# Kernel tuning notes

Measured on AMD Instinct MI355X. Metric: run time of the kernel, lower is better.

## Reference

```python
import jax, jax.numpy as jnp
import numpy as np
from jax import lax

B, L, D_MODEL = 4, 512, 256
N_LAYERS = 6
EXPAND = 2
D_INNER = EXPAND * D_MODEL  # 512
D_STATE = 16
D_CONV = 4
DT_RANK = (D_MODEL + 15) // 16  # 16
EPS = 1e-5


def silu(x):
    return x * jax.nn.sigmoid(x)


def rmsnorm(x, w):
    var = jnp.mean(x * x, axis=-1, keepdims=True)
    return x * lax.rsqrt(var + EPS) * w


def setup_inputs() -> dict:
    key = jax.random.key(0)
    ks = jax.random.split(key, 12)
    s = lambda *sh: 0.02
    inp = {
        "x": jax.random.normal(ks[0], (B, L, D_MODEL), dtype=jnp.float32),
        "norm_w": jnp.ones((N_LAYERS, D_MODEL), jnp.float32),
        "W_in": jax.random.normal(ks[1], (N_LAYERS, 2 * D_INNER, D_MODEL), jnp.float32) * 0.02,
        "b_in": jnp.zeros((N_LAYERS, 2 * D_INNER), jnp.float32),
        "conv_w": jax.random.normal(ks[2], (N_LAYERS, D_INNER, D_CONV), jnp.float32) * 0.2,
        "W_x": jax.random.normal(ks[3], (N_LAYERS, DT_RANK + 2 * D_STATE, D_INNER), jnp.float32) * 0.02,
        "dt_w": jax.random.normal(ks[4], (N_LAYERS, D_INNER, DT_RANK), jnp.float32) * 0.1,
        "dt_b": jax.random.uniform(ks[5], (N_LAYERS, D_INNER), jnp.float32, -4.0, -2.0),
        "A_log": jnp.log(jnp.broadcast_to(jnp.arange(1, D_STATE + 1, dtype=jnp.float32), (N_LAYERS, D_INNER, D_STATE))),
        "D": jnp.ones((N_LAYERS, D_INNER), jnp.float32),
        "W_out": jax.random.normal(ks[6], (N_LAYERS, D_MODEL, D_INNER), jnp.float32) * 0.02,
        "b_out": jnp.zeros((N_LAYERS, D_MODEL), jnp.float32),
    }
    return inp


def mamba_block(x, W_in, b_in, conv_w, W_x, dt_w, dt_b, A_log, D, W_out, b_out):
    # input projection -> (B, L, 2*d_inner)
    xz = jnp.einsum("bld,ed->ble", x, W_in) + b_in
    xin, z = xz[..., :D_INNER], xz[..., D_INNER:]
    # depthwise causal conv over time (groups = d_inner, left pad d_conv-1)
    xc = lax.conv_general_dilated(
        xin.transpose(0, 2, 1),            # (B, C, L)
        conv_w[:, None, :],                # (C, 1, K)
        window_strides=(1,),
        padding=[(D_CONV - 1, 0)],
        feature_group_count=D_INNER,
        dimension_numbers=("NCH", "OIH", "NCH"),
    ).transpose(0, 2, 1)
    u = silu(xc)                           # (B, L, d_inner)
    # data-dependent dt, B, C
    xdbc = jnp.einsum("bld,rd->blr", u, W_x)
    dt = xdbc[..., :DT_RANK]
    Bm = xdbc[..., DT_RANK:DT_RANK + D_STATE]
    Cm = xdbc[..., DT_RANK + D_STATE:]
    delta = jax.nn.softplus(jnp.einsum("blr,dr->bld", dt, dt_w) + dt_b)
    A = -jnp.exp(A_log)                    # (d_inner, d_state)
    dA = jnp.exp(jnp.einsum("bld,dn->bldn", delta, A))
    dBu = jnp.einsum("bld,bln->bldn", delta * u, Bm)
    # selective scan over time
    def step(h, inp):
        dA_t, dBu_t, C_t = inp
        h = dA_t * h + dBu_t               # (B, d_inner, d_state)
        y_t = jnp.einsum("bdn,bn->bd", h, C_t)
        return h, y_t
    h0 = jnp.zeros((B, D_INNER, D_STATE), x.dtype)
    _, ys = lax.scan(step, h0, (dA.transpose(1, 0, 2, 3), dBu.transpose(1, 0, 2, 3), Cm.transpose(1, 0, 2)))
    y = ys.transpose(1, 0, 2) + u * D      # skip connection D*u
    y = y * silu(z)
    return jnp.einsum("bld,md->blm", y, W_out) + b_out


def reference(x, norm_w, W_in, b_in, conv_w, W_x, dt_w, dt_b, A_log, D, W_out, b_out):
    for i in range(N_LAYERS):
        x = x + mamba_block(rmsnorm(x, norm_w[i]), W_in[i], b_in[i], conv_w[i], W_x[i], dt_w[i], dt_b[i], A_log[i], D[i], W_out[i], b_out[i])
    return x
```

## Files before the change

### kernel.cpp

```cpp
#include <hip/hip_runtime.h>
#include <hip/hip_bf16.h>

#define B_SZ 4
#define L_SZ 512
#define D_MODEL 256
#define D_INNER 512
#define D_STATE 16
#define DT_RANK 16
#define N_LAYERS 6
#define BL (B_SZ * L_SZ)

typedef __bf16 bf16_t;
typedef __bf16 bf16x8 __attribute__((ext_vector_type(8)));
typedef __bf16 bf16x4 __attribute__((ext_vector_type(4)));
typedef float  f32x4  __attribute__((ext_vector_type(4)));

__device__ __forceinline__ float row_allreduce16(float x)
{
    int v;
    v = __builtin_amdgcn_mov_dpp(__float_as_int(x), 0x121, 0xf, 0xf, true);
    x += __int_as_float(v);
    v = __builtin_amdgcn_mov_dpp(__float_as_int(x), 0x122, 0xf, 0xf, true);
    x += __int_as_float(v);
    v = __builtin_amdgcn_mov_dpp(__float_as_int(x), 0x124, 0xf, 0xf, true);
    x += __int_as_float(v);
    v = __builtin_amdgcn_mov_dpp(__float_as_int(x), 0x128, 0xf, 0xf, true);
    x += __int_as_float(v);
    return x;
}

__global__ __launch_bounds__(256) void cast3_kernel(
    const float* __restrict__ s0, const float* __restrict__ s1,
    const float* __restrict__ s2, bf16_t* __restrict__ dst,
    int n0, int n1, int n2)
{
    int i = blockIdx.x * 256 + threadIdx.x;
    const float* s; int off;
    if (i < n0)            { s = s0; off = i; }
    else if (i < n0 + n1)  { s = s1; off = i - n0; }
    else if (i < n0+n1+n2) { s = s2; off = i - n0 - n1; }
    else return;
    const float4 v = *(const float4*)(s + (size_t)off * 4);
    bf16x4 o;
    o[0] = (bf16_t)v.x; o[1] = (bf16_t)v.y;
    o[2] = (bf16_t)v.z; o[3] = (bf16_t)v.w;
    *(bf16x4*)(dst + (size_t)i * 4) = o;
}

__global__ __launch_bounds__(256) void rmsnorm_kernel(
    const float* __restrict__ x, const float* __restrict__ w,
    bf16_t* __restrict__ o)
{
    int row  = blockIdx.x * 4 + (threadIdx.x >> 6);
    int lane = threadIdx.x & 63;
    const float4 v = *(const float4*)(x + (size_t)row * D_MODEL + lane * 4);
    float ss = v.x * v.x + v.y * v.y + v.z * v.z + v.w * v.w;
    #pragma unroll
    for (int off = 32; off; off >>= 1) ss += __shfl_xor(ss, off);
    float rs = rsqrtf(ss * (1.f / D_MODEL) + 1e-5f);
    const float4 wv = *(const float4*)(w + lane * 4);
    bf16x4 ov;
    ov[0] = (bf16_t)(v.x * rs * wv.x);
    ov[1] = (bf16_t)(v.y * rs * wv.y);
    ov[2] = (bf16_t)(v.z * rs * wv.z);
    ov[3] = (bf16_t)(v.w * rs * wv.w);
    *(bf16x4*)(o + (size_t)row * D_MODEL + lane * 4) = ov;
}

__global__ __launch_bounds__(256) void win_kernel(
    const bf16_t* __restrict__ A,
    const bf16_t* __restrict__ Bw,
    const float* __restrict__ bias,
    float* __restrict__ C,
    float* __restrict__ Z)
{
    constexpr int K = 256, BK = 64;
    __shared__ bf16_t As[64][K + 8];
    __shared__ bf16_t Bs[64][BK + 8];

    const int tid  = threadIdx.x;
    const int wave = tid >> 6, lane = tid & 63;
    const int wm = wave >> 1, wn = wave & 1;
    const int lm = lane & 15, quad = lane >> 4;
    const int m0 = blockIdx.y * 64, n0 = blockIdx.x * 64;

    #pragma unroll
    for (int i = tid; i < 64 * (K / 8); i += 256) {
        int r = i >> 5, c8 = i & 31;
        *(bf16x8*)&As[r][c8 * 8] =
            *(const bf16x8*)(A + (size_t)(m0 + r) * K + c8 * 8);
    }

    f32x4 acc[2][2] = {};
    for (int k0 = 0; k0 < K; k0 += BK) {
        #pragma unroll
        for (int i = tid; i < 64 * (BK / 8); i += 256) {
            int r = i >> 3, c8 = i & 7;
            *(bf16x8*)&Bs[r][c8 * 8] =
                *(const bf16x8*)(Bw + (size_t)(n0 + r) * K + k0 + c8 * 8);
        }
        __syncthreads();
        #pragma unroll
        for (int ks = 0; ks < 2; ++ks) {
            bf16x8 af[2], bfr[2];
            #pragma unroll
            for (int i = 0; i < 2; ++i)
                af[i] = *(const bf16x8*)&As[wm * 32 + i * 16 + lm][k0 + ks * 32 + quad * 8];
            #pragma unroll
            for (int j = 0; j < 2; ++j)
                bfr[j] = *(const bf16x8*)&Bs[wn * 32 + j * 16 + lm][ks * 32 + quad * 8];
            #pragma unroll
            for (int i = 0; i < 2; ++i)
                #pragma unroll
                for (int j = 0; j < 2; ++j)
                    acc[i][j] = __builtin_amdgcn_mfma_f32_16x16x32_bf16(
                        af[i], bfr[j], acc[i][j], 0, 0, 0);
        }
        __syncthreads();
    }

    if (n0 >= D_INNER) {
        #pragma unroll
        for (int i = 0; i < 2; ++i) {
            int rowbase = m0 + wm * 32 + i * 16 + quad * 4;
            #pragma unroll
            for (int j = 0; j < 2; ++j) {
                int col = n0 + wn * 32 + j * 16 + lm;
                float4 o;
                #pragma unroll
                for (int r = 0; r < 4; ++r) {
                    float v = acc[i][j][r] + bias[col];
                    ((float*)&o)[r] = v / (1.f + __expf(-v));
                }
                *(float4*)(Z + (size_t)(col - D_INNER) * BL + rowbase) = o;
            }
        }
        return;
    }

    #pragma unroll
    for (int i = 0; i < 2; ++i) {
        #pragma unroll
        for (int j = 0; j < 2; ++j) {
            int col = n0 + wn * 32 + j * 16 + lm;
            #pragma unroll
            for (int r = 0; r < 4; ++r) {
                int rowm = m0 + wm * 32 + i * 16 + quad * 4 + r;
                C[(size_t)rowm * D_INNER + col] = acc[i][j][r] + bias[col];
            }
        }
    }
}

template<int WM, int WN, int TM_T, int TN_T>
__global__ __launch_bounds__(64 * WM * WN) void gemm_wout(
    const bf16_t* __restrict__ A, int lda,
    const bf16_t* __restrict__ Bw, int ldb,
    const float* __restrict__ bias,
    const float* __restrict__ R, int ldr,
    float* __restrict__ C, int ldc, int K)
{
    constexpr int BK = 64;
    constexpr int BM = WM * TM_T * 16;
    constexpr int BN = WN * TN_T * 16;
    constexpr int NT = 64 * WM * WN;
    constexpr int LDK = BK + 8;
    __shared__ bf16_t As[BM][LDK];
    __shared__ bf16_t Bs[BN][LDK];

    const int tid  = threadIdx.x;
    const int wave = tid >> 6, lane = tid & 63;
    const int wm = wave / WN, wn = wave % WN;
    const int lm = lane & 15, quad = lane >> 4;
    const int m0 = blockIdx.y * BM, n0 = blockIdx.x * BN;

    f32x4 acc[TM_T][TN_T] = {};

    for (int k0 = 0; k0 < K; k0 += BK) {
        #pragma unroll
        for (int i = tid; i < BM * (BK / 8); i += NT) {
            int r = i >> 3, c8 = i & 7;
            *(bf16x8*)&As[r][c8 * 8] =
                *(const bf16x8*)(A + (size_t)(m0 + r) * lda + k0 + c8 * 8);
        }
        #pragma unroll
        for (int i = tid; i < BN * (BK / 8); i += NT) {
            int r = i >> 3, c8 = i & 7;
            *(bf16x8*)&Bs[r][c8 * 8] =
                *(const bf16x8*)(Bw + (size_t)(n0 + r) * ldb + k0 + c8 * 8);
        }
        __syncthreads();
        #pragma unroll
        for (int ks = 0; ks < BK / 32; ++ks) {
            bf16x8 af[TM_T], bfr[TN_T];
            #pragma unroll
            for (int i = 0; i < TM_T; ++i)
                af[i] = *(const bf16x8*)&As[wm * TM_T * 16 + i * 16 + lm][ks * 32 + quad * 8];
            #pragma unroll
            for (int j = 0; j < TN_T; ++j)
                bfr[j] = *(const bf16x8*)&Bs[wn * TN_T * 16 + j * 16 + lm][ks * 32 + quad * 8];
            #pragma unroll
            for (int i = 0; i < TM_T; ++i)
                #pragma unroll
                for (int j = 0; j < TN_T; ++j)
                    acc[i][j] = __builtin_amdgcn_mfma_f32_16x16x32_bf16(
                        af[i], bfr[j], acc[i][j], 0, 0, 0);
        }
        __syncthreads();
    }

    #pragma unroll
    for (int i = 0; i < TM_T; ++i) {
        #pragma unroll
        for (int j = 0; j < TN_T; ++j) {
            int col = n0 + wn * TN_T * 16 + j * 16 + lm;
            #pragma unroll
            for (int r = 0; r < 4; ++r) {
                int rowm = m0 + wm * TM_T * 16 + i * 16 + quad * 4 + r;
                C[(size_t)rowm * ldc + col] =
                    acc[i][j][r] + bias[col] + R[(size_t)rowm * ldr + col];
            }
        }
    }
}

__global__ __launch_bounds__(256) void wx_conv_kernel(
    const float* __restrict__ xzx,
    const float* __restrict__ cw,
    const bf16_t* __restrict__ Bw,
    const float* __restrict__ dt_w,
    const float* __restrict__ dt_b,
    float* __restrict__ uT,
    float* __restrict__ xdbcT,
    float* __restrict__ deltaT)
{
    constexpr int K = 512;
    __shared__ float  xs[19][516];
    __shared__ bf16_t us[16][520];
    __shared__ f32x4  part[4][3][64];
    __shared__ float  dtt[16][17];

    const int tid  = threadIdx.x;
    const int wave = tid >> 6, lane = tid & 63;
    const int lm = lane & 15, quad = lane >> 4;
    const int m0 = blockIdx.x * 16;

    for (int q = tid; q < 19 * 128; q += 256) {
        int rx = q >> 7, c4 = (q & 127) * 4;
        int mr = m0 - 3 + rx;
        float4 v = make_float4(0.f, 0.f, 0.f, 0.f);
        if (mr >= 0) v = *(const float4*)(xzx + (size_t)mr * K + c4);
        *(float4*)&xs[rx][c4] = v;
    }
    __syncthreads();

    #pragma unroll
    for (int it = 0; it < 8; ++it) {
        int item = tid + it * 256;
        int d = item >> 2, rg = item & 3;
        const float4 wv = *(const float4*)(cw + d * 4);
        float4 o;
        #pragma unroll
        for (int e = 0; e < 4; ++e) {
            int ro = rg * 4 + e;
            int t  = (m0 + ro) & (L_SZ - 1);
            float a = wv.w * xs[ro + 3][d];
            if (t >= 1) a += wv.z * xs[ro + 2][d];
            if (t >= 2) a += wv.y * xs[ro + 1][d];
            if (t >= 3) a += wv.x * xs[ro + 0][d];
            a = a / (1.f + __expf(-a));
            ((float*)&o)[e] = a;
            us[ro][d] = (bf16_t)a;
        }
        *(float4*)(uT + (size_t)d * BL + m0 + rg * 4) = o;
    }
    __syncthreads();

    f32x4 acc[3] = {};
    const int kb = wave * 128 + quad * 8;
    #pragma unroll
    for (int ks = 0; ks < 4; ++ks) {
        int k0 = kb + ks * 32;
        bf16x8 af = *(const bf16x8*)&us[lm][k0];
        #pragma unroll
        for (int j = 0; j < 3; ++j) {
            bf16x8 bfr = *(const bf16x8*)(Bw + (size_t)(j * 16 + lm) * K + k0);
            acc[j] = __builtin_amdgcn_mfma_f32_16x16x32_bf16(af, bfr, acc[j], 0, 0, 0);
        }
    }
    #pragma unroll
    for (int j = 0; j < 3; ++j) part[wave][j][lane] = acc[j];
    __syncthreads();

    if (tid < 192) {
        int j = tid >> 6, l = tid & 63;
        f32x4 s = part[0][j][l];
        s += part[1][j][l];
        s += part[2][j][l];
        s += part[3][j][l];
        int col = j * 16 + (l & 15);
        float4 v = make_float4(s[0], s[1], s[2], s[3]);
        *(float4*)(xdbcT + (size_t)col * BL + m0 + (l >> 4) * 4) = v;
        if (j == 0) {
            #pragma unroll
            for (int e = 0; e < 4; ++e)
                dtt[(l >> 4) * 4 + e][l & 15] = s[e];
        }
    }
    __syncthreads();

    #pragma unroll
    for (int it = 0; it < 8; ++it) {
        int item = tid + it * 256;
        int d = item >> 2, tg = item & 3;
        const float4 w0 = *(const float4*)(dt_w + (size_t)d * 16 + 0);
        const float4 w1 = *(const float4*)(dt_w + (size_t)d * 16 + 4);
        const float4 w2 = *(const float4*)(dt_w + (size_t)d * 16 + 8);
        const float4 w3 = *(const float4*)(dt_w + (size_t)d * 16 + 12);
        const float bdt = dt_b[d];
        float4 o;
        #pragma unroll
        for (int e = 0; e < 4; ++e) {
            int t = tg * 4 + e;
            float a = bdt;
            a += dtt[t][0]  * w0.x + dtt[t][1]  * w0.y + dtt[t][2]  * w0.z + dtt[t][3]  * w0.w;
            a += dtt[t][4]  * w1.x + dtt[t][5]  * w1.y + dtt[t][6]  * w1.z + dtt[t][7]  * w1.w;
            a += dtt[t][8]  * w2.x + dtt[t][9]  * w2.y + dtt[t][10] * w2.z + dtt[t][11] * w2.w;
            a += dtt[t][12] * w3.x + dtt[t][13] * w3.y + dtt[t][14] * w3.z + dtt[t][15] * w3.w;
            ((float*)&o)[e] = (a > 20.f) ? a : __logf(1.f + __expf(a));
        }
        *(float4*)(deltaT + (size_t)d * BL + m0 + tg * 4) = o;
    }
}

__global__ __launch_bounds__(1024, 4) void scan_kernel(
    const float* __restrict__ xdbcT,
    const float* __restrict__ deltaT,
    const float* __restrict__ uT,
    const float* __restrict__ szT,
    const float* __restrict__ A_log,
    const float* __restrict__ Dv,
    bf16_t* __restrict__ y)
{
    constexpr int TC = 32;
    constexpr int NW = L_SZ / TC;

    int blk  = blockIdx.x;
    int b    = blk >> 7;
    int dg   = blk & 127;
    int wave = threadIdx.x >> 6;
    int lane = threadIdx.x & 63;
    int d    = dg * 4 + (lane >> 4);
    int n    = lane & 15;

    __shared__ float lds_Ap[NW][64];
    __shared__ float lds_he[NW][64];

    float Adn = -__expf(A_log[d * D_STATE + n]);
    int r0 = b * L_SZ + wave * TC;

    const float* Brow = xdbcT  + (size_t)(DT_RANK + n) * BL;
    const float* Crow = xdbcT  + (size_t)(DT_RANK + D_STATE + n) * BL;
    const float* drow = deltaT + (size_t)d * BL;
    const float* urow = uT     + (size_t)d * BL;
    const float* zrow = szT    + (size_t)d * BL;

    {
        float h = 0.f, P = 1.f;
        #pragma unroll
        for (int j4 = 0; j4 < 8; ++j4) {
            int rb = r0 + j4 * 4;
            f32x4 dl = *(const f32x4*)(drow + rb);
            f32x4 Bv = *(const f32x4*)(Brow + rb);
            f32x4 uv = *(const f32x4*)(urow + rb);
            #pragma unroll
            for (int k = 0; k < 4; ++k) {
                float dA = __expf(dl[k] * Adn);
                h = dA * h + dl[k] * uv[k] * Bv[k];
                P *= dA;
            }
        }
        lds_Ap[wave][lane] = P;
        lds_he[wave][lane] = h;
    }
    __syncthreads();

    float H = 0.f;
    for (int j = 0; j < wave; ++j)
        H = lds_Ap[j][lane] * H + lds_he[j][lane];

    float Dd = Dv[d];
    float h = H;
    #pragma unroll
    for (int g = 0; g < 2; ++g) {
        float py[16];
        #pragma unroll
        for (int j4 = 0; j4 < 4; ++j4) {
            int rb = r0 + g * 16 + j4 * 4;
            f32x4 dl = *(const f32x4*)(drow + rb);
            f32x4 Bv = *(const f32x4*)(Brow + rb);
            f32x4 uv = *(const f32x4*)(urow + rb);
            f32x4 Cc = *(const f32x4*)(Crow + rb);
            #pragma unroll
            for (int k = 0; k < 4; ++k) {
                float dA = __expf(dl[k] * Adn);
                h = dA * h + dl[k] * uv[k] * Bv[k];
                py[j4 * 4 + k] = h * Cc[k];
            }
        }
        #pragma unroll
        for (int j = 0; j < 16; ++j)
            py[j] = row_allreduce16(py[j]);
        if (n == 0) {
            #pragma unroll
            for (int j4 = 0; j4 < 4; ++j4) {
                int rb = r0 + g * 16 + j4 * 4;
                f32x4 uv = *(const f32x4*)(urow + rb);
                f32x4 sz = *(const f32x4*)(zrow + rb);
                #pragma unroll
                for (int k = 0; k < 4; ++k) {
                    int row = rb + k;
                    y[(size_t)row * D_INNER + d] =
                        (bf16_t)((py[j4*4+k] + uv[k] * Dd) * sz[k]);
                }
            }
        }
    }
}

extern "C" void kernel_launch(void* const* d_in, const int* in_sizes, int n_in,
                              void* d_out, int out_size, void* d_ws, size_t ws_size,
                              hipStream_t stream)
{
    const float* x_in   = (const float*)d_in[0];
    const float* norm_w = (const float*)d_in[1];
    const float* W_in   = (const float*)d_in[2];
    const float* b_in   = (const float*)d_in[3];
    const float* conv_w = (const float*)d_in[4];
    const float* W_x    = (const float*)d_in[5];
    const float* dt_w   = (const float*)d_in[6];
    const float* dt_b   = (const float*)d_in[7];
    const float* A_log  = (const float*)d_in[8];
    const float* Dv     = (const float*)d_in[9];
    const float* W_out  = (const float*)d_in[10];
    const float* b_out  = (const float*)d_in[11];
    float* out = (float*)d_out;

    float* ws     = (float*)d_ws;
    float* xz     = ws;
    float* uT     = xz     + BL * D_INNER;
    float* szT    = uT     + D_INNER * BL;
    float* xdbcT  = szT    + D_INNER * BL;
    float* deltaT = xdbcT  + 48 * BL;
    bf16_t* bws   = (bf16_t*)(deltaT + D_INNER * BL);
    bf16_t* xn_bf = bws;
    bf16_t* y_bf  = xn_bf + BL * D_MODEL;
    bf16_t* Wi_bf = y_bf  + BL * D_INNER;
    bf16_t* Wx_bf = Wi_bf + N_LAYERS * 2 * D_INNER * D_MODEL;
    bf16_t* Wo_bf = Wx_bf + N_LAYERS * 48 * D_INNER;

    {
        int n0 = N_LAYERS * 2 * D_INNER * D_MODEL / 4;
        int n1 = N_LAYERS * 48 * D_INNER / 4;
        int n2 = N_LAYERS * D_MODEL * D_INNER / 4;
        cast3_kernel<<<(n0 + n1 + n2 + 255) / 256, 256, 0, stream>>>(
            W_in, W_x, W_out, Wi_bf, n0, n1, n2);
    }

    for (int i = 0; i < N_LAYERS; ++i) {
        const float* xcur = (i == 0) ? x_in : out;

        rmsnorm_kernel<<<BL / 4, 256, 0, stream>>>(xcur, norm_w + i * D_MODEL, xn_bf);

        win_kernel<<<dim3(1024 / 64, 2048 / 64), 256, 0, stream>>>(
            xn_bf, Wi_bf + (size_t)i * 2 * D_INNER * D_MODEL,
            b_in + i * 2 * D_INNER, xz, szT);

        wx_conv_kernel<<<BL / 16, 256, 0, stream>>>(
            xz, conv_w + i * D_INNER * 4,
            Wx_bf + (size_t)i * 48 * D_INNER,
            dt_w + (size_t)i * D_INNER * DT_RANK, dt_b + i * D_INNER,
            uT, xdbcT, deltaT);

        scan_kernel<<<512, 1024, 0, stream>>>(
            xdbcT, deltaT, uT, szT,
            A_log + (size_t)i * D_INNER * D_STATE, Dv + i * D_INNER, y_bf);

        gemm_wout<2, 2, 2, 2><<<dim3(256 / 64, 2048 / 64), 256, 0, stream>>>(
            y_bf, D_INNER, Wo_bf + (size_t)i * D_MODEL * D_INNER, D_INNER,
            b_out + i * D_MODEL, xcur, D_MODEL, out, D_MODEL, D_INNER);
    }
}
```

Before: 558.3 us.

## Fuse next layer's RMSNorm into W_out GEMM epilogue with full-row tiles

Restructures the output projection GEMM so each block computes full 256-wide rows (BM=16, BN=256), letting the epilogue add bias and residual, reduce the row sum of squares across waves, and write both the fp32 residual stream and the next layer's normalized bf16 input. This removes the separate rmsnorm launch per layer (except the first) and its extra read of the residual. The narrower M tile means every block reloads the whole W_out slice, and the grid changes to 128 blocks of 16 rows, which may lower MFMA efficiency. On the last layer it computes an unused normalized output.

```diff
diff --git a/kernel.cpp b/kernel.cpp
--- a/kernel.cpp
+++ b/kernel.cpp
@@ -152,74 +152,86 @@
     }
 }
 
-template<int WM, int WN, int TM_T, int TN_T>
-__global__ __launch_bounds__(64 * WM * WN) void gemm_wout(
-    const bf16_t* __restrict__ A, int lda,
-    const bf16_t* __restrict__ Bw, int ldb,
+__global__ __launch_bounds__(256) void gemm_wout_norm(
+    const bf16_t* __restrict__ A,
+    const bf16_t* __restrict__ Bw,
     const float* __restrict__ bias,
-    const float* __restrict__ R, int ldr,
-    float* __restrict__ C, int ldc, int K)
-{
-    constexpr int BK = 64;
-    constexpr int BM = WM * TM_T * 16;
-    constexpr int BN = WN * TN_T * 16;
-    constexpr int NT = 64 * WM * WN;
-    constexpr int LDK = BK + 8;
+    const float* __restrict__ R,
+    const float* __restrict__ nw,
+    float* __restrict__ C,
+    bf16_t* __restrict__ Xn)
+{
+    constexpr int K = 512, BK = 64, BM = 16, BN = 256, LDK = BK + 8;
     __shared__ bf16_t As[BM][LDK];
     __shared__ bf16_t Bs[BN][LDK];
+    __shared__ float rsum[BM][5];
 
     const int tid  = threadIdx.x;
     const int wave = tid >> 6, lane = tid & 63;
-    const int wm = wave / WN, wn = wave % WN;
     const int lm = lane & 15, quad = lane >> 4;
-    const int m0 = blockIdx.y * BM, n0 = blockIdx.x * BN;
-
-    f32x4 acc[TM_T][TN_T] = {};
-
+    const int m0 = blockIdx.x * BM;
+
+    f32x4 acc[4] = {};
     for (int k0 = 0; k0 < K; k0 += BK) {
-        #pragma unroll
-        for (int i = tid; i < BM * (BK / 8); i += NT) {
-            int r = i >> 3, c8 = i & 7;
+        if (tid < BM * (BK / 8)) {
+            int r = tid >> 3, c8 = tid & 7;
             *(bf16x8*)&As[r][c8 * 8] =
-                *(const bf16x8*)(A + (size_t)(m0 + r) * lda + k0 + c8 * 8);
-        }
-        #pragma unroll
-        for (int i = tid; i < BN * (BK / 8); i += NT) {
+                *(const bf16x8*)(A + (size_t)(m0 + r) * K + k0 + c8 * 8);
+        }
+        #pragma unroll
+        for (int i = tid; i < BN * (BK / 8); i += 256) {
             int r = i >> 3, c8 = i & 7;
             *(bf16x8*)&Bs[r][c8 * 8] =
-                *(const bf16x8*)(Bw + (size_t)(n0 + r) * ldb + k0 + c8 * 8);
+                *(const bf16x8*)(Bw + (size_t)r * K + k0 + c8 * 8);
         }
         __syncthreads();
         #pragma unroll
-        for (int ks = 0; ks < BK / 32; ++ks) {
-            bf16x8 af[TM_T], bfr[TN_T];
-            #pragma unroll
-            for (int i = 0; i < TM_T; ++i)
-                af[i] = *(const bf16x8*)&As[wm * TM_T * 16 + i * 16 + lm][ks * 32 + quad * 8];
-            #pragma unroll
-            for (int j = 0; j < TN_T; ++j)
-                bfr[j] = *(const bf16x8*)&Bs[wn * TN_T * 16 + j * 16 + lm][ks * 32 + quad * 8];
-            #pragma unroll
-            for (int i = 0; i < TM_T; ++i)
-                #pragma unroll
-                for (int j = 0; j < TN_T; ++j)
-                    acc[i][j] = __builtin_amdgcn_mfma_f32_16x16x32_bf16(
-                        af[i], bfr[j], acc[i][j], 0, 0, 0);
+        for (int ks = 0; ks < 2; ++ks) {
+            bf16x8 af = *(const bf16x8*)&As[lm][ks * 32 + quad * 8];
+            #pragma unroll
+            for (int j = 0; j < 4; ++j) {
+                bf16x8 bfr = *(const bf16x8*)&Bs[wave * 64 + j * 16 + lm][ks * 32 + quad * 8];
+                acc[j] = __builtin_amdgcn_mfma_f32_16x16x32_bf16(af, bfr, acc[j], 0, 0, 0);
+            }
         }
         __syncthreads();
     }
 
-    #pragma unroll
-    for (int i = 0; i < TM_T; ++i) {
-        #pragma unroll
-        for (int j = 0; j < TN_T; ++j) {
-            int col = n0 + wn * TN_T * 16 + j * 16 + lm;
-            #pragma unroll
-            for (int r = 0; r < 4; ++r) {
-                int rowm = m0 + wm * TM_T * 16 + i * 16 + quad * 4 + r;
-                C[(size_t)rowm * ldc + col] =
-                    acc[i][j][r] + bias[col] + R[(size_t)rowm * ldr + col];
-            }
+    float vv[4][4];
+    #pragma unroll
+    for (int j = 0; j < 4; ++j) {
+        int col = wave * 64 + j * 16 + lm;
+        float bj = bias[col];
+        #pragma unroll
+        for (int r = 0; r < 4; ++r) {
+            int row = m0 + quad * 4 + r;
+            vv[j][r] = acc[j][r] + bj + R[(size_t)row * D_MODEL + col];
+        }
+    }
+    #pragma unroll
+    for (int r = 0; r < 4; ++r) {
+        float p = vv[0][r] * vv[0][r] + vv[1][r] * vv[1][r]
+                + vv[2][r] * vv[2][r] + vv[3][r] * vv[3][r];
+        p = row_allreduce16(p);
+        if (lm == 0) rsum[quad * 4 + r][wave] = p;
+    }
+    __syncthreads();
+    float rs[4];
+    #pragma unroll
+    for (int r = 0; r < 4; ++r) {
+        int lr = quad * 4 + r;
+        float tot = rsum[lr][0] + rsum[lr][1] + rsum[lr][2] + rsum[lr][3];
+        rs[r] = rsqrtf(tot * (1.f / D_MODEL) + 1e-5f);
+    }
+    #pragma unroll
+    for (int j = 0; j < 4; ++j) {
+        int col = wave * 64 + j * 16 + lm;
+        float wj = nw[col];
+        #pragma unroll
+        for (int r = 0; r < 4; ++r) {
+            int row = m0 + quad * 4 + r;
+            C[(size_t)row * D_MODEL + col] = vv[j][r];
+            Xn[(size_t)row * D_MODEL + col] = (bf16_t)(vv[j][r] * rs[r] * wj);
         }
     }
 }
@@ -467,10 +479,10 @@
             W_in, W_x, W_out, Wi_bf, n0, n1, n2);
     }
 
+    rmsnorm_kernel<<<BL / 4, 256, 0, stream>>>(x_in, norm_w, xn_bf);
+
     for (int i = 0; i < N_LAYERS; ++i) {
         const float* xcur = (i == 0) ? x_in : out;
-
-        rmsnorm_kernel<<<BL / 4, 256, 0, stream>>>(xcur, norm_w + i * D_MODEL, xn_bf);
 
         win_kernel<<<dim3(1024 / 64, 2048 / 64), 256, 0, stream>>>(
             xn_bf, Wi_bf + (size_t)i * 2 * D_INNER * D_MODEL,
@@ -486,8 +498,9 @@
             xdbcT, deltaT, uT, szT,
             A_log + (size_t)i * D_INNER * D_STATE, Dv + i * D_INNER, y_bf);
 
-        gemm_wout<2, 2, 2, 2><<<dim3(256 / 64, 2048 / 64), 256, 0, stream>>>(
-            y_bf, D_INNER, Wo_bf + (size_t)i * D_MODEL * D_INNER, D_INNER,
-            b_out + i * D_MODEL, xcur, D_MODEL, out, D_MODEL, D_INNER);
-    }
-}
+        const float* nw_next = norm_w + (size_t)((i + 1) % N_LAYERS) * D_MODEL;
+        gemm_wout_norm<<<BL / 16, 256, 0, stream>>>(
+            y_bf, Wo_bf + (size_t)i * D_MODEL * D_INNER,
+            b_out + i * D_MODEL, xcur, nw_next, out, xn_bf);
+    }
+}
```

New measurement: 572.2 us. 1.02x slower.
